# Kernel tuning notes

Hardware: AMD Instinct MI355X
Metric: run time of the kernel (lower is better)

## Reference

```python
import jax, jax.numpy as jnp
import numpy as np

DIM = 1024
NUM_HEADS = 16
HEAD_DIM = DIM // NUM_HEADS
SCALE = HEAD_DIM ** -0.5


def apply_rope(x):
    # x: [B, H, S, D]; rotate pairs (x1, x2) split as first/second half of D
    S, D = x.shape[-2], x.shape[-1]
    pos = jnp.arange(S, dtype=jnp.float32)[:, None]                      # [S, 1]
    freqs = jnp.exp(jnp.arange(0, D, 2, dtype=jnp.float32) * (-np.log(10000.0) / D))  # [D/2]
    emb = pos * freqs                                                    # [S, D/2]
    cos = jnp.cos(emb)[None, None, :, :].astype(x.dtype)                 # [1,1,S,D/2]
    sin = jnp.sin(emb)[None, None, :, :].astype(x.dtype)
    x1, x2 = jnp.split(x, 2, axis=-1)
    return jnp.concatenate([x1 * cos - x2 * sin, x1 * sin + x2 * cos], axis=-1)


def setup_inputs() -> dict:
    key = jax.random.key(0)
    ks = jax.random.split(key, 6)
    B, S = 2, 2048
    x = jax.random.normal(ks[0], (B, S, DIM), dtype=jnp.float32)
    # torch nn.Linear weights: [out_features, in_features]
    w_std = DIM ** -0.5
    wq = jax.random.normal(ks[1], (DIM, DIM), dtype=jnp.float32) * w_std
    wk = jax.random.normal(ks[2], (DIM, DIM), dtype=jnp.float32) * w_std
    wv = jax.random.normal(ks[3], (DIM, DIM), dtype=jnp.float32) * w_std
    wo = jax.random.normal(ks[4], (DIM, DIM), dtype=jnp.float32) * w_std
    wo_b = jax.random.normal(ks[5], (DIM,), dtype=jnp.float32) * 0.01
    return {"x": x, "wq": wq, "wk": wk, "wv": wv, "wo": wo, "wo_b": wo_b}


def reference(x, wq, wk, wv, wo, wo_b):
    B, S, _ = x.shape
    def proj(w):
        # y = x @ w.T -> [B, S, dim] -> [B, H, S, head_dim]
        y = jnp.einsum('bsd,ed->bse', x, w)
        return y.reshape(B, S, NUM_HEADS, HEAD_DIM).transpose(0, 2, 1, 3)
    q = apply_rope(proj(wq))
    k = apply_rope(proj(wk))
    v = proj(wv)
    attn = jnp.einsum('bhqd,bhkd->bhqk', q, k) * SCALE   # [B,H,S,S]
    attn = jax.nn.softmax(attn, axis=-1)                 # dropout is identity in eval
    out = jnp.einsum('bhqk,bhkd->bhqd', attn, v)         # [B,H,S,D]
    out = out.transpose(0, 2, 1, 3).reshape(B, S, DIM)
    return jnp.einsum('bsd,ed->bse', out, wo) + wo_b
```

## Files before the change

### kernel.cpp

```cpp
#include <hip/hip_runtime.h>
#include <hip/hip_bf16.h>

typedef __attribute__((ext_vector_type(8))) short s16x8;
typedef __attribute__((ext_vector_type(4))) short s16x4;
typedef __attribute__((ext_vector_type(4))) float f32x4;

#define SEQ 2048
#define NB 2
#define NH 16
#define HD 64
#define DIM 1024
#define MR (NB * SEQ)
#define NT (SEQ / 64)
#define QSC 0.18033688011112042f

__device__ __forceinline__ unsigned short f2b(float f) {
    unsigned u = __float_as_uint(f);
    u += 0x7fffu + ((u >> 16) & 1u);
    return (unsigned short)(u >> 16);
}

__device__ __forceinline__ unsigned pk2(float a, float b) {
    unsigned r;
    asm("v_cvt_pk_bf16_f32 %0, %1, %2" : "=v"(r) : "v"(a), "v"(b));
    return r;
}

__device__ __forceinline__ s16x8 mk8(unsigned a, unsigned b, unsigned c, unsigned d) {
    union { unsigned u[4]; s16x8 v; } x;
    x.u[0] = a; x.u[1] = b; x.u[2] = c; x.u[3] = d;
    return x.v;
}

__device__ __forceinline__ s16x8 cat8(s16x4 a, s16x4 b) {
    union { s16x4 h[2]; s16x8 v; } x;
    x.h[0] = a; x.h[1] = b;
    return x.v;
}

__device__ __forceinline__ void gl_lds16(const unsigned short* g, unsigned short* l) {
    __builtin_amdgcn_global_load_lds(
        (const __attribute__((address_space(1))) void*)g,
        (__attribute__((address_space(3))) void*)l, 16, 0, 0);
}

__device__ __forceinline__ unsigned ldsoff(const void* p) {
    return (unsigned)(size_t)(const __attribute__((address_space(3))) void*)p;
}

__device__ __forceinline__ void cast4(const float* __restrict__ src, unsigned short* __restrict__ dst, int i) {
    float4 v = reinterpret_cast<const float4*>(src)[i];
    ushort4 o;
    o.x = f2b(v.x); o.y = f2b(v.y); o.z = f2b(v.z); o.w = f2b(v.w);
    reinterpret_cast<ushort4*>(dst)[i] = o;
}

__global__ __launch_bounds__(256) void prep_kernel(
    const float* __restrict__ x, const float* __restrict__ wq, const float* __restrict__ wk,
    const float* __restrict__ wv, const float* __restrict__ wo,
    unsigned short* __restrict__ xb, unsigned short* __restrict__ wqkv,
    unsigned short* __restrict__ wwo, float2* __restrict__ tab)
{
    int b = blockIdx.x, t = threadIdx.x;
    if (b < 4096)       cast4(x,  xb,                 b * 256 + t);
    else if (b < 5120)  cast4(wq, wqkv,               (b - 4096) * 256 + t);
    else if (b < 6144)  cast4(wk, wqkv + DIM * DIM,   (b - 5120) * 256 + t);
    else if (b < 7168)  cast4(wv, wqkv + 2 * DIM * DIM, (b - 6144) * 256 + t);
    else if (b < 8192)  cast4(wo, wwo,                (b - 7168) * 256 + t);
    else {
        int i = (b - 8192) * 256 + t;
        int pos = i >> 5, fi = i & 31;
        float freq = expf((float)fi * (-9.210340371976184f / 32.0f));
        float emb = (float)pos * freq;
        tab[i] = make_float2(cosf(emb), sinf(emb));
    }
}

template <int EPI>
__global__ __launch_bounds__(256) void gemm_mw(
    const unsigned short* __restrict__ A,
    const unsigned short* __restrict__ Bw,
    const float2* __restrict__ tab,
    unsigned short* __restrict__ qw,
    unsigned short* __restrict__ kw,
    unsigned short* __restrict__ vw,
    float* __restrict__ out,
    const float* __restrict__ bias)
{
    __shared__ unsigned short As[2][4096];
    __shared__ unsigned short Bs[2][4096];
    const int t = threadIdx.x;
    const int wid = t >> 6, lane = t & 63;
    const int wr = wid >> 1, wc = wid & 1;
    const int lo = lane & 15, hi = lane >> 4;
    const int wg = blockIdx.x;
    const int xcd = wg & 7, bi = wg >> 3;
    const int by = xcd * 4 + (bi & 3);
    const int bx = bi >> 2;
    const int m0 = by * 128, n0 = bx * 128;

    const unsigned short* agp = A + (long)(m0 + (t >> 2)) * DIM + (t & 3) * 8;
    const unsigned short* bgp = Bw + (long)(n0 + (t >> 2)) * DIM + (t & 3) * 8;
    unsigned short* alds = &As[0][0] + wid * 512;
    unsigned short* blds = &Bs[0][0] + wid * 512;

#define STG(buf, k0) {                                        \
        gl_lds16(agp + (k0), alds + (buf) * 4096);            \
        gl_lds16(agp + (k0) + 64 * DIM, alds + (buf) * 4096 + 2048); \
        gl_lds16(bgp + (k0), blds + (buf) * 4096);            \
        gl_lds16(bgp + (k0) + 64 * DIM, blds + (buf) * 4096 + 2048); }

    f32x4 acc[4][4] = {};
    STG(0, 0)
    STG(1, 32)

    for (int kt = 0; kt < 32; ++kt) {
        const int cb = kt & 1;
        if (kt < 31) { asm volatile("s_waitcnt vmcnt(4)" ::: "memory"); }
        else         { asm volatile("s_waitcnt vmcnt(0)" ::: "memory"); }
        __builtin_amdgcn_sched_barrier(0);
        __builtin_amdgcn_s_barrier();
        __builtin_amdgcn_sched_barrier(0);
        s16x8 af[4], bf[4];
#pragma unroll
        for (int i = 0; i < 4; ++i)
            af[i] = *reinterpret_cast<const s16x8*>(&As[cb][(wr * 64 + i * 16 + lo) * 32 + hi * 8]);
#pragma unroll
        for (int j = 0; j < 4; ++j)
            bf[j] = *reinterpret_cast<const s16x8*>(&Bs[cb][(wc * 64 + j * 16 + lo) * 32 + hi * 8]);
        asm volatile("s_waitcnt lgkmcnt(0)" ::: "memory");
        __builtin_amdgcn_sched_barrier(0);
        if (kt + 2 < 32) {
            __builtin_amdgcn_s_barrier();
            __builtin_amdgcn_sched_barrier(0);
            STG(cb, (kt + 2) * 32)
        }
        __builtin_amdgcn_s_setprio(1);
#pragma unroll
        for (int i = 0; i < 4; ++i)
#pragma unroll
            for (int j = 0; j < 4; ++j)
                acc[i][j] = __builtin_amdgcn_mfma_f32_16x16x32_bf16(af[i], bf[j], acc[i][j], 0, 0, 0);
        __builtin_amdgcn_s_setprio(0);
    }
#undef STG

    const int rowb = m0 + wr * 64;
    const int colb = n0 + wc * 64;
    if (EPI == 0) {
#pragma unroll
        for (int ai = 0; ai < 4; ++ai) {
#pragma unroll
            for (int cp = 0; cp < 2; ++cp) {
                f32x4 v1 = acc[ai][cp];
                f32x4 v2 = acc[ai][cp + 2];
                int e = colb + cp * 16 + lo;
                int which = e >> 10;
                int eh = e & 1023;
                int h = eh >> 6, d = eh & 63;
                unsigned short* dst = (which == 0) ? qw : ((which == 1) ? kw : vw);
                float qs = (which == 0) ? QSC : 1.0f;
#pragma unroll
                for (int r = 0; r < 4; ++r) {
                    int m = rowb + ai * 16 + hi * 4 + r;
                    int b = m >> 11, pos = m & (SEQ - 1);
                    long off = (((long)(b * NH + h)) * SEQ + pos) * HD;
                    if (which == 2) {
                        dst[off + d]      = f2b(v1[r]);
                        dst[off + d + 32] = f2b(v2[r]);
                    } else {
                        float2 cs = tab[pos * 32 + d];
                        dst[off + d]      = f2b((v1[r] * cs.x - v2[r] * cs.y) * qs);
                        dst[off + d + 32] = f2b((v1[r] * cs.y + v2[r] * cs.x) * qs);
                    }
                }
            }
        }
    } else {
#pragma unroll
        for (int ai = 0; ai < 4; ++ai)
#pragma unroll
            for (int cj = 0; cj < 4; ++cj) {
                int n = colb + cj * 16 + lo;
                float bv = bias[n];
#pragma unroll
                for (int r = 0; r < 4; ++r) {
                    int m = rowb + ai * 16 + hi * 4 + r;
                    out[(long)m * DIM + n] = acc[ai][cj][r] + bv;
                }
            }
    }
}

template <int EPI>
__global__ __launch_bounds__(64, 2) void gemm_async(
    const unsigned short* __restrict__ A,
    const unsigned short* __restrict__ Bw,
    const float2* __restrict__ tab,
    unsigned short* __restrict__ qw,
    unsigned short* __restrict__ kw,
    unsigned short* __restrict__ vw,
    float* __restrict__ out,
    const float* __restrict__ bias)
{
    __shared__ unsigned short As[2 * 2048];
    __shared__ unsigned short Bs[2 * 4096];
    const int lane = threadIdx.x & 63;
    const int lo = lane & 15, hi = lane >> 4;
    const int wg = blockIdx.x;
    const int xcd = wg & 7, bi = wg >> 3;
    const int bx = bi >> 3;
    const int by = xcd * 8 + (bi & 7);
    const int m0 = by * 64, n0 = bx * 128;

    const unsigned short* agp = A + (long)(m0 + (lane >> 2)) * DIM + (lane & 3) * 8;
    const unsigned short* bgp = Bw + (long)(n0 + (lane >> 2)) * DIM + (lane & 3) * 8;

    f32x4 acc[4][8] = {};

#define STG(buf, k0) {                                       \
        unsigned short* al = &As[(buf) * 2048];              \
        unsigned short* bl = &Bs[(buf) * 4096];              \
        _Pragma("unroll") for (int s = 0; s < 4; ++s)        \
            gl_lds16(agp + (k0) + (long)s * 16 * DIM, al + s * 512); \
        _Pragma("unroll") for (int s = 0; s < 8; ++s)        \
            gl_lds16(bgp + (k0) + (long)s * 16 * DIM, bl + s * 512); }

    STG(0, 0)
    STG(1, 32)

    for (int kt = 0; kt < 32; ++kt) {
        const int cb = kt & 1;
        if (kt < 31) { asm volatile("s_waitcnt vmcnt(12)" ::: "memory"); }
        else         { asm volatile("s_waitcnt vmcnt(0)" ::: "memory"); }
        __builtin_amdgcn_sched_barrier(0);
        s16x8 af[4], bf[8];
#pragma unroll
        for (int i = 0; i < 4; ++i)
            af[i] = *reinterpret_cast<const s16x8*>(&As[cb * 2048 + (i * 16 + lo) * 32 + hi * 8]);
#pragma unroll
        for (int j = 0; j < 8; ++j)
            bf[j] = *reinterpret_cast<const s16x8*>(&Bs[cb * 4096 + (j * 16 + lo) * 32 + hi * 8]);
        asm volatile("s_waitcnt lgkmcnt(0)" ::: "memory");
        __builtin_amdgcn_sched_barrier(0);
        if (kt + 2 < 32) STG(cb, (kt + 2) * 32)
        __builtin_amdgcn_sched_barrier(0);
        __builtin_amdgcn_s_setprio(1);
#pragma unroll
        for (int i = 0; i < 4; ++i)
#pragma unroll
            for (int j = 0; j < 8; ++j)
                acc[i][j] = __builtin_amdgcn_mfma_f32_16x16x32_bf16(af[i], bf[j], acc[i][j], 0, 0, 0);
        __builtin_amdgcn_s_setprio(0);
    }
#undef STG

    if (EPI == 0) {
#pragma unroll
        for (int ai = 0; ai < 4; ++ai) {
#pragma unroll
            for (int g = 0; g < 2; ++g) {
#pragma unroll
                for (int cp = 0; cp < 2; ++cp) {
                    f32x4 v1 = acc[ai][g * 4 + cp];
                    f32x4 v2 = acc[ai][g * 4 + cp + 2];
                    int e = n0 + g * 64 + cp * 16 + lo;
                    int which = e >> 10;
                    int eh = e & 1023;
                    int h = eh >> 6, d = eh & 63;
                    unsigned short* dst = (which == 0) ? qw : ((which == 1) ? kw : vw);
                    float qs = (which == 0) ? QSC : 1.0f;
#pragma unroll
                    for (int r = 0; r < 4; ++r) {
                        int m = m0 + ai * 16 + hi * 4 + r;
                        int b = m >> 11, pos = m & (SEQ - 1);
                        long off = (((long)(b * NH + h)) * SEQ + pos) * HD;
                        if (which == 2) {
                            dst[off + d]      = f2b(v1[r]);
                            dst[off + d + 32] = f2b(v2[r]);
                        } else {
                            float2 cs = tab[pos * 32 + d];
                            dst[off + d]      = f2b((v1[r] * cs.x - v2[r] * cs.y) * qs);
                            dst[off + d + 32] = f2b((v1[r] * cs.y + v2[r] * cs.x) * qs);
                        }
                    }
                }
            }
        }
    } else {
#pragma unroll
        for (int ai = 0; ai < 4; ++ai)
#pragma unroll
            for (int bj = 0; bj < 8; ++bj) {
                int n = n0 + bj * 16 + lo;
                float bv = bias[n];
#pragma unroll
                for (int r = 0; r < 4; ++r) {
                    int m = m0 + ai * 16 + hi * 4 + r;
                    out[(long)m * DIM + n] = acc[ai][bj][r] + bv;
                }
            }
    }
}

__global__ __launch_bounds__(256) void flash_attn(
    const unsigned short* __restrict__ qw,
    const unsigned short* __restrict__ kw,
    const unsigned short* __restrict__ vw,
    unsigned short* __restrict__ ao)
{
    __shared__ __align__(16) unsigned char smem[33792];
    const int t = threadIdx.x;
    const int w = t >> 6, lane = t & 63;
    const int lo = lane & 15, hi = lane >> 4;
    const int wg = blockIdx.x;
    const int swz = (wg & 7) * 128 + (wg >> 3);
    const int bh = swz >> 5;
    const int q0 = (swz & 31) * 64;
    const unsigned short* qh = qw + (long)bh * SEQ * HD;
    const unsigned short* kh = kw + (long)bh * SEQ * HD;
    const unsigned short* vh = vw + (long)bh * SEQ * HD;

    s16x8 qf[4][2];
#pragma unroll
    for (int qt = 0; qt < 4; ++qt)
#pragma unroll
        for (int ds = 0; ds < 2; ++ds)
            qf[qt][ds] = *reinterpret_cast<const s16x8*>(
                qh + (long)(q0 + qt * 16 + lo) * HD + ds * 32 + hi * 8);
    asm volatile("s_waitcnt vmcnt(0)" ::: "memory");

    unsigned char* wbase = smem + w * 8192;
    const int kr0 = lane >> 3, ks0 = (lane & 7) ^ (kr0 & 7);
    const int kr1 = 8 + (lane >> 3), ks1 = (lane & 7) ^ (kr1 & 7);
    const unsigned short* ksrc0 = kh + (16 * w + kr0) * HD + ks0 * 8;
    const unsigned short* ksrc1 = kh + (16 * w + kr1) * HD + ks1 * 8;
    const int c0 = lane, c1 = 64 + lane;
    const int kl0 = ((c0 >> 3 >> 2) << 2) | ((c0 >> 1) & 3);
    const int dd0 = (((c0 >> 3) & 3) << 4) | ((c0 & 1) << 3);
    const int kl1 = ((c1 >> 3 >> 2) << 2) | ((c1 >> 1) & 3);
    const int dd1 = (((c1 >> 3) & 3) << 4) | ((c1 & 1) << 3);
    const unsigned short* vsrc0 = vh + (16 * w + kl0) * HD + dd0;
    const unsigned short* vsrc1 = vh + (16 * w + kl1) * HD + dd1;

#define STAGE(buf, kb) {                                              \
        unsigned short* d_ = (unsigned short*)(wbase + (buf) * 4096); \
        gl_lds16(ksrc0 + (kb) * HD, d_);                              \
        gl_lds16(ksrc1 + (kb) * HD, d_ + 512);                        \
        gl_lds16(vsrc0 + (kb) * HD, d_ + 1024);                       \
        gl_lds16(vsrc1 + (kb) * HD, d_ + 1536); }

    const int kro0 = lo * 128 + ((hi ^ (lo & 7)) << 4);
    const int kro1 = lo * 128 + (((4 + hi) ^ (lo & 7)) << 4);
    const unsigned vtb0 = ldsoff(wbase) + 2048 + hi * 512 + lo * 8;

    f32x4 od[4][4] = {};
    f32x4 lr = {0.f, 0.f, 0.f, 0.f};

    STAGE(0, 0)
    STAGE(1, 64)

    constexpr int NT2 = NT / 2;
    for (int i2 = 0; i2 < NT2; ++i2) {
        const bool more = (i2 + 1 < NT2);
        asm volatile("s_waitcnt vmcnt(4)" ::: "memory");
        s16x8 kf0 = *reinterpret_cast<const s16x8*>(wbase + kro0);
        s16x8 kf1 = *reinterpret_cast<const s16x8*>(wbase + kro1);
        s16x4 va0, va1, va2, va3;
        asm volatile("ds_read_b64_tr_b16 %0, %1"            : "=v"(va0) : "v"(vtb0));
        asm volatile("ds_read_b64_tr_b16 %0, %1 offset:128" : "=v"(va1) : "v"(vtb0));
        asm volatile("ds_read_b64_tr_b16 %0, %1 offset:256" : "=v"(va2) : "v"(vtb0));
        asm volatile("ds_read_b64_tr_b16 %0, %1 offset:384" : "=v"(va3) : "v"(vtb0));
        asm volatile("s_waitcnt lgkmcnt(0)" ::: "memory");
        __builtin_amdgcn_sched_barrier(0);

        f32x4 sc[4] = {};
        __builtin_amdgcn_s_setprio(1);
#pragma unroll
        for (int qt = 0; qt < 4; ++qt)
            sc[qt] = __builtin_amdgcn_mfma_f32_16x16x32_bf16(kf0, qf[qt][0], sc[qt], 0, 0, 0);
#pragma unroll
        for (int qt = 0; qt < 4; ++qt)
            sc[qt] = __builtin_amdgcn_mfma_f32_16x16x32_bf16(kf1, qf[qt][1], sc[qt], 0, 0, 0);
        __builtin_amdgcn_s_setprio(0);
        if (more) STAGE(0, (2 * i2 + 2) * 64)

        unsigned u01[4], u23[4];
#pragma unroll
        for (int qt = 0; qt < 4; ++qt) {
            float p0 = exp2f(sc[qt][0]), p1 = exp2f(sc[qt][1]);
            float p2 = exp2f(sc[qt][2]), p3 = exp2f(sc[qt][3]);
            lr[qt] += (p0 + p1) + (p2 + p3);
            u01[qt] = pk2(p0, p1); u23[qt] = pk2(p2, p3);
        }

        if (more) { asm volatile("s_waitcnt vmcnt(4)" ::: "memory"); }
        else      { asm volatile("s_waitcnt vmcnt(0)" ::: "memory"); }
        s16x8 kg0 = *reinterpret_cast<const s16x8*>(wbase + 4096 + kro0);
        s16x8 kg1 = *reinterpret_cast<const s16x8*>(wbase + 4096 + kro1);
        s16x4 vb0, vb1, vb2, vb3;
        const unsigned vtb1 = vtb0 + 4096;
        asm volatile("ds_read_b64_tr_b16 %0, %1"            : "=v"(vb0) : "v"(vtb1));
        asm volatile("ds_read_b64_tr_b16 %0, %1 offset:128" : "=v"(vb1) : "v"(vtb1));
        asm volatile("ds_read_b64_tr_b16 %0, %1 offset:256" : "=v"(vb2) : "v"(vtb1));
        asm volatile("ds_read_b64_tr_b16 %0, %1 offset:384" : "=v"(vb3) : "v"(vtb1));
        asm volatile("s_waitcnt lgkmcnt(0)" ::: "memory");
        __builtin_amdgcn_sched_barrier(0);

        f32x4 sd[4] = {};
        __builtin_amdgcn_s_setprio(1);
#pragma unroll
        for (int qt = 0; qt < 4; ++qt)
            sd[qt] = __builtin_amdgcn_mfma_f32_16x16x32_bf16(kg0, qf[qt][0], sd[qt], 0, 0, 0);
#pragma unroll
        for (int qt = 0; qt < 4; ++qt)
            sd[qt] = __builtin_amdgcn_mfma_f32_16x16x32_bf16(kg1, qf[qt][1], sd[qt], 0, 0, 0);
        __builtin_amdgcn_s_setprio(0);
        if (more) STAGE(1, (2 * i2 + 3) * 64)

        s16x8 pf8[4];
#pragma unroll
        for (int qt = 0; qt < 4; ++qt) {
            float p0 = exp2f(sd[qt][0]), p1 = exp2f(sd[qt][1]);
            float p2 = exp2f(sd[qt][2]), p3 = exp2f(sd[qt][3]);
            lr[qt] += (p0 + p1) + (p2 + p3);
            pf8[qt] = mk8(u01[qt], u23[qt], pk2(p0, p1), pk2(p2, p3));
        }
        s16x8 vf80 = cat8(va0, vb0), vf81 = cat8(va1, vb1);
        s16x8 vf82 = cat8(va2, vb2), vf83 = cat8(va3, vb3);

        __builtin_amdgcn_s_setprio(1);
#pragma unroll
        for (int qt = 0; qt < 4; ++qt) {
            od[0][qt] = __builtin_amdgcn_mfma_f32_16x16x32_bf16(vf80, pf8[qt], od[0][qt], 0, 0, 0);
            od[1][qt] = __builtin_amdgcn_mfma_f32_16x16x32_bf16(vf81, pf8[qt], od[1][qt], 0, 0, 0);
            od[2][qt] = __builtin_amdgcn_mfma_f32_16x16x32_bf16(vf82, pf8[qt], od[2][qt], 0, 0, 0);
            od[3][qt] = __builtin_amdgcn_mfma_f32_16x16x32_bf16(vf83, pf8[qt], od[3][qt], 0, 0, 0);
        }
        __builtin_amdgcn_s_setprio(0);
    }
#undef STAGE

#pragma unroll
    for (int qt = 0; qt < 4; ++qt) {
        lr[qt] += __shfl_xor(lr[qt], 16);
        lr[qt] += __shfl_xor(lr[qt], 32);
    }
    __syncthreads();
    float* red = reinterpret_cast<float*>(smem);
    float* ldl = reinterpret_cast<float*>(smem + 32768);
    if (lane < 16) {
#pragma unroll
        for (int qt = 0; qt < 4; ++qt) ldl[w * 64 + qt * 16 + lane] = lr[qt];
    }

    const int b = bh >> 4, h = bh & 15;
    const int ql = w * 16 + (lane >> 2);
    const int qc = ql & 7;
    float linv = 0.f;
#pragma unroll
    for (int p = 0; p < 2; ++p) {
        if (p) __syncthreads();
#pragma unroll
        for (int dtp = 0; dtp < 2; ++dtp) {
#pragma unroll
            for (int qt = 0; qt < 4; ++qt) {
                int q = qt * 16 + lo;
                int quad = ((dtp << 2) + hi) ^ (lo & 7);
                *reinterpret_cast<f32x4*>(red + w * 2048 + q * 32 + quad * 4) = od[p * 2 + dtp][qt];
            }
        }
        __syncthreads();
        float s0[8] = {0.f, 0.f, 0.f, 0.f, 0.f, 0.f, 0.f, 0.f};
#pragma unroll
        for (int w2 = 0; w2 < 4; ++w2)
#pragma unroll
            for (int k = 0; k < 2; ++k) {
                int quad = (((lane & 3) << 1) + k) ^ qc;
                f32x4 v = *reinterpret_cast<const f32x4*>(red + w2 * 2048 + ql * 32 + quad * 4);
#pragma unroll
                for (int j = 0; j < 4; ++j) s0[k * 4 + j] += v[j];
            }
        if (p == 0)
            linv = 1.f / (ldl[ql] + ldl[64 + ql] + ldl[128 + ql] + ldl[192 + ql]);
        unsigned uu[4];
#pragma unroll
        for (int k2 = 0; k2 < 4; ++k2)
            uu[k2] = pk2(s0[2 * k2] * linv, s0[2 * k2 + 1] * linv);
        int4 ov;
        ov.x = uu[0]; ov.y = uu[1]; ov.z = uu[2]; ov.w = uu[3];
        *reinterpret_cast<int4*>(ao + ((long)(b * SEQ + q0 + ql)) * DIM +
                                 h * 64 + p * 32 + (lane & 3) * 8) = ov;
    }
}

extern "C" void kernel_launch(void* const* d_in, const int* in_sizes, int n_in,
                              void* d_out, int out_size, void* d_ws, size_t ws_size,
                              hipStream_t stream) {
    const float* x   = (const float*)d_in[0];
    const float* wq  = (const float*)d_in[1];
    const float* wk  = (const float*)d_in[2];
    const float* wv  = (const float*)d_in[3];
    const float* wo  = (const float*)d_in[4];
    const float* wob = (const float*)d_in[5];

    char* ws = (char*)d_ws;
    unsigned short* xb   = (unsigned short*)(ws);
    unsigned short* wqkv = (unsigned short*)(ws + 8388608);
    unsigned short* wwo  = (unsigned short*)(ws + 14680064);
    unsigned short* qw   = (unsigned short*)(ws + 16777216);
    unsigned short* kw   = (unsigned short*)(ws + 25165824);
    unsigned short* vw   = (unsigned short*)(ws + 33554432);
    unsigned short* ao   = (unsigned short*)(ws + 41943040);
    float2* tab          = (float2*)(ws + 50331648);

    prep_kernel<<<8448, 256, 0, stream>>>(x, wq, wk, wv, wo, xb, wqkv, wwo, tab);

    gemm_mw<0><<<768, 256, 0, stream>>>(xb, wqkv, tab, qw, kw, vw, nullptr, nullptr);
    flash_attn<<<1024, 256, 0, stream>>>(qw, kw, vw, ao);
    gemm_async<1><<<512, 64, 0, stream>>>(ao, wwo, nullptr, nullptr, nullptr, nullptr,
                                          (float*)d_out, wob);
}
```

Measured before the change: 127.2 us.

## Halve flash-attention query tile to 32 rows and double the grid

Each attention workgroup now handles 32 query rows instead of 64, and the launch grid doubles to 2048 blocks. The goal is more parallelism and fewer registers per wave (smaller Q fragments and accumulators), which may help occupancy. The cross-wave reduction epilogue is rewritten as a single pass with one barrier, using a new swizzled LDS layout. The cost is that each K/V tile loaded from memory is reused across half as many queries, so K/V global traffic doubles.

```diff
diff --git a/kernel.cpp b/kernel.cpp
--- a/kernel.cpp
+++ b/kernel.cpp
@@ -314,16 +314,16 @@
     const int w = t >> 6, lane = t & 63;
     const int lo = lane & 15, hi = lane >> 4;
     const int wg = blockIdx.x;
-    const int swz = (wg & 7) * 128 + (wg >> 3);
-    const int bh = swz >> 5;
-    const int q0 = (swz & 31) * 64;
+    const int swz = (wg & 7) * 256 + (wg >> 3);
+    const int bh = swz >> 6;
+    const int q0 = (swz & 63) * 32;
     const unsigned short* qh = qw + (long)bh * SEQ * HD;
     const unsigned short* kh = kw + (long)bh * SEQ * HD;
     const unsigned short* vh = vw + (long)bh * SEQ * HD;
 
-    s16x8 qf[4][2];
-#pragma unroll
-    for (int qt = 0; qt < 4; ++qt)
+    s16x8 qf[2][2];
+#pragma unroll
+    for (int qt = 0; qt < 2; ++qt)
 #pragma unroll
         for (int ds = 0; ds < 2; ++ds)
             qf[qt][ds] = *reinterpret_cast<const s16x8*>(
@@ -354,8 +354,8 @@
     const int kro1 = lo * 128 + (((4 + hi) ^ (lo & 7)) << 4);
     const unsigned vtb0 = ldsoff(wbase) + 2048 + hi * 512 + lo * 8;
 
-    f32x4 od[4][4] = {};
-    f32x4 lr = {0.f, 0.f, 0.f, 0.f};
+    f32x4 od[4][2] = {};
+    float lr0 = 0.f, lr1 = 0.f;
 
     STAGE(0, 0)
     STAGE(1, 64)
@@ -374,23 +374,23 @@
         asm volatile("s_waitcnt lgkmcnt(0)" ::: "memory");
         __builtin_amdgcn_sched_barrier(0);
 
-        f32x4 sc[4] = {};
+        f32x4 sc[2] = {};
         __builtin_amdgcn_s_setprio(1);
 #pragma unroll
-        for (int qt = 0; qt < 4; ++qt)
+        for (int qt = 0; qt < 2; ++qt)
             sc[qt] = __builtin_amdgcn_mfma_f32_16x16x32_bf16(kf0, qf[qt][0], sc[qt], 0, 0, 0);
 #pragma unroll
-        for (int qt = 0; qt < 4; ++qt)
+        for (int qt = 0; qt < 2; ++qt)
             sc[qt] = __builtin_amdgcn_mfma_f32_16x16x32_bf16(kf1, qf[qt][1], sc[qt], 0, 0, 0);
         __builtin_amdgcn_s_setprio(0);
         if (more) STAGE(0, (2 * i2 + 2) * 64)
 
-        unsigned u01[4], u23[4];
-#pragma unroll
-        for (int qt = 0; qt < 4; ++qt) {
+        unsigned u01[2], u23[2];
+#pragma unroll
+        for (int qt = 0; qt < 2; ++qt) {
             float p0 = exp2f(sc[qt][0]), p1 = exp2f(sc[qt][1]);
             float p2 = exp2f(sc[qt][2]), p3 = exp2f(sc[qt][3]);
-            lr[qt] += (p0 + p1) + (p2 + p3);
+            if (qt == 0) lr0 += (p0 + p1) + (p2 + p3); else lr1 += (p0 + p1) + (p2 + p3);
             u01[qt] = pk2(p0, p1); u23[qt] = pk2(p2, p3);
         }
 
@@ -407,23 +407,23 @@
         asm volatile("s_waitcnt lgkmcnt(0)" ::: "memory");
         __builtin_amdgcn_sched_barrier(0);
 
-        f32x4 sd[4] = {};
+        f32x4 sd[2] = {};
         __builtin_amdgcn_s_setprio(1);
 #pragma unroll
-        for (int qt = 0; qt < 4; ++qt)
+        for (int qt = 0; qt < 2; ++qt)
             sd[qt] = __builtin_amdgcn_mfma_f32_16x16x32_bf16(kg0, qf[qt][0], sd[qt], 0, 0, 0);
 #pragma unroll
-        for (int qt = 0; qt < 4; ++qt)
+        for (int qt = 0; qt < 2; ++qt)
             sd[qt] = __builtin_amdgcn_mfma_f32_16x16x32_bf16(kg1, qf[qt][1], sd[qt], 0, 0, 0);
         __builtin_amdgcn_s_setprio(0);
         if (more) STAGE(1, (2 * i2 + 3) * 64)
 
-        s16x8 pf8[4];
-#pragma unroll
-        for (int qt = 0; qt < 4; ++qt) {
+        s16x8 pf8[2];
+#pragma unroll
+        for (int qt = 0; qt < 2; ++qt) {
             float p0 = exp2f(sd[qt][0]), p1 = exp2f(sd[qt][1]);
             float p2 = exp2f(sd[qt][2]), p3 = exp2f(sd[qt][3]);
-            lr[qt] += (p0 + p1) + (p2 + p3);
+            if (qt == 0) lr0 += (p0 + p1) + (p2 + p3); else lr1 += (p0 + p1) + (p2 + p3);
             pf8[qt] = mk8(u01[qt], u23[qt], pk2(p0, p1), pk2(p2, p3));
         }
         s16x8 vf80 = cat8(va0, vb0), vf81 = cat8(va1, vb1);
@@ -431,7 +431,7 @@
 
         __builtin_amdgcn_s_setprio(1);
 #pragma unroll
-        for (int qt = 0; qt < 4; ++qt) {
+        for (int qt = 0; qt < 2; ++qt) {
             od[0][qt] = __builtin_amdgcn_mfma_f32_16x16x32_bf16(vf80, pf8[qt], od[0][qt], 0, 0, 0);
             od[1][qt] = __builtin_amdgcn_mfma_f32_16x16x32_bf16(vf81, pf8[qt], od[1][qt], 0, 0, 0);
             od[2][qt] = __builtin_amdgcn_mfma_f32_16x16x32_bf16(vf82, pf8[qt], od[2][qt], 0, 0, 0);
@@ -441,57 +441,45 @@
     }
 #undef STAGE
 
-#pragma unroll
-    for (int qt = 0; qt < 4; ++qt) {
-        lr[qt] += __shfl_xor(lr[qt], 16);
-        lr[qt] += __shfl_xor(lr[qt], 32);
-    }
-    __syncthreads();
+    lr0 += __shfl_xor(lr0, 16); lr0 += __shfl_xor(lr0, 32);
+    lr1 += __shfl_xor(lr1, 16); lr1 += __shfl_xor(lr1, 32);
     float* red = reinterpret_cast<float*>(smem);
     float* ldl = reinterpret_cast<float*>(smem + 32768);
     if (lane < 16) {
-#pragma unroll
-        for (int qt = 0; qt < 4; ++qt) ldl[w * 64 + qt * 16 + lane] = lr[qt];
-    }
+        ldl[w * 32 + lane] = lr0;
+        ldl[w * 32 + 16 + lane] = lr1;
+    }
+#pragma unroll
+    for (int dt = 0; dt < 4; ++dt)
+#pragma unroll
+        for (int qt = 0; qt < 2; ++qt) {
+            int q = qt * 16 + lo;
+            int quad = (dt * 4 + hi) ^ lo;
+            *reinterpret_cast<f32x4*>(red + w * 2048 + q * 64 + quad * 4) = od[dt][qt];
+        }
+    __syncthreads();
 
     const int b = bh >> 4, h = bh & 15;
-    const int ql = w * 16 + (lane >> 2);
-    const int qc = ql & 7;
-    float linv = 0.f;
-#pragma unroll
-    for (int p = 0; p < 2; ++p) {
-        if (p) __syncthreads();
-#pragma unroll
-        for (int dtp = 0; dtp < 2; ++dtp) {
-#pragma unroll
-            for (int qt = 0; qt < 4; ++qt) {
-                int q = qt * 16 + lo;
-                int quad = ((dtp << 2) + hi) ^ (lo & 7);
-                *reinterpret_cast<f32x4*>(red + w * 2048 + q * 32 + quad * 4) = od[p * 2 + dtp][qt];
-            }
-        }
-        __syncthreads();
-        float s0[8] = {0.f, 0.f, 0.f, 0.f, 0.f, 0.f, 0.f, 0.f};
-#pragma unroll
-        for (int w2 = 0; w2 < 4; ++w2)
-#pragma unroll
-            for (int k = 0; k < 2; ++k) {
-                int quad = (((lane & 3) << 1) + k) ^ qc;
-                f32x4 v = *reinterpret_cast<const f32x4*>(red + w2 * 2048 + ql * 32 + quad * 4);
-#pragma unroll
-                for (int j = 0; j < 4; ++j) s0[k * 4 + j] += v[j];
-            }
-        if (p == 0)
-            linv = 1.f / (ldl[ql] + ldl[64 + ql] + ldl[128 + ql] + ldl[192 + ql]);
-        unsigned uu[4];
-#pragma unroll
-        for (int k2 = 0; k2 < 4; ++k2)
-            uu[k2] = pk2(s0[2 * k2] * linv, s0[2 * k2 + 1] * linv);
-        int4 ov;
-        ov.x = uu[0]; ov.y = uu[1]; ov.z = uu[2]; ov.w = uu[3];
-        *reinterpret_cast<int4*>(ao + ((long)(b * SEQ + q0 + ql)) * DIM +
-                                 h * 64 + p * 32 + (lane & 3) * 8) = ov;
-    }
+    const int ql = t >> 3;
+    const int c = t & 7;
+    float s0[8] = {0.f, 0.f, 0.f, 0.f, 0.f, 0.f, 0.f, 0.f};
+#pragma unroll
+    for (int w2 = 0; w2 < 4; ++w2)
+#pragma unroll
+        for (int k = 0; k < 2; ++k) {
+            int phys = (2 * c + k) ^ (ql & 15);
+            f32x4 v = *reinterpret_cast<const f32x4*>(red + w2 * 2048 + ql * 64 + phys * 4);
+#pragma unroll
+            for (int j = 0; j < 4; ++j) s0[k * 4 + j] += v[j];
+        }
+    float linv = 1.f / (ldl[ql] + ldl[32 + ql] + ldl[64 + ql] + ldl[96 + ql]);
+    unsigned uu[4];
+#pragma unroll
+    for (int k2 = 0; k2 < 4; ++k2)
+        uu[k2] = pk2(s0[2 * k2] * linv, s0[2 * k2 + 1] * linv);
+    int4 ov;
+    ov.x = uu[0]; ov.y = uu[1]; ov.z = uu[2]; ov.w = uu[3];
+    *reinterpret_cast<int4*>(ao + ((long)(b * SEQ + q0 + ql)) * DIM + h * 64 + c * 8) = ov;
 }
 
 extern "C" void kernel_launch(void* const* d_in, const int* in_sizes, int n_in,
@@ -517,7 +505,7 @@
     prep_kernel<<<8448, 256, 0, stream>>>(x, wq, wk, wv, wo, xb, wqkv, wwo, tab);
 
     gemm_mw<0><<<768, 256, 0, stream>>>(xb, wqkv, tab, qw, kw, vw, nullptr, nullptr);
-    flash_attn<<<1024, 256, 0, stream>>>(qw, kw, vw, ao);
+    flash_attn<<<2048, 256, 0, stream>>>(qw, kw, vw, ao);
     gemm_async<1><<<512, 64, 0, stream>>>(ao, wwo, nullptr, nullptr, nullptr, nullptr,
                                           (float*)d_out, wob);
 }
```

Measured after the change: 133.9 us. +5.3%, slower.
